# Optimization experiments

Measured on AMD Instinct MI355X. Metric: run time of the kernel, lower is better.

## Reference

```python
import jax, jax.numpy as jnp
import numpy as np

B, T, F = 256, 512, 64
H1, H2, OUT = 100, 128, 19


def setup_inputs() -> dict:
    key = jax.random.key(0)
    ks = jax.random.split(key, 6)
    s = 0.05  # small init so relu cell activation stays stable over 512 steps
    return {
        "x":  jax.random.normal(ks[0], (B, T, F), jnp.float32),
        "W1": jax.random.normal(ks[1], (F, 4 * H1), jnp.float32) * s,
        "U1": jax.random.normal(ks[2], (H1, 4 * H1), jnp.float32) * s,
        "b1": jnp.zeros((4 * H1,), jnp.float32),
        "W2": jax.random.normal(ks[3], (H1, 4 * H2), jnp.float32) * s,
        "U2": jax.random.normal(ks[4], (H2, 4 * H2), jnp.float32) * s,
        "b2": jnp.zeros((4 * H2,), jnp.float32),
        "Wd": jax.random.normal(ks[5], (H2, OUT), jnp.float32) * s,
        "bd": jnp.zeros((OUT,), jnp.float32),
    }


def _lstm_relu(x, W, U, b):
    """Keras LSTM with activation=relu, recurrent_activation=sigmoid.
    x: [B,T,F]. Returns full hidden sequence [B,T,H]. Gate order i,f,g,o."""
    H = U.shape[0]
    xproj = jnp.einsum('btf,fj->btj', x, W) + b  # [B,T,4H], input gemm hoisted out of scan

    def step(carry, xt):
        h, c = carry
        z = xt + h @ U                            # [B,4H]
        i, f, g, o = jnp.split(z, 4, axis=-1)
        i = jax.nn.sigmoid(i)
        f = jax.nn.sigmoid(f)
        g = jax.nn.relu(g)
        o = jax.nn.sigmoid(o)
        c = f * c + i * g
        h = o * jax.nn.relu(c)
        return (h, c), h

    h0 = jnp.zeros((x.shape[0], H), x.dtype)
    c0 = jnp.zeros_like(h0)
    _, hs = jax.lax.scan(step, (h0, c0), jnp.swapaxes(xproj, 0, 1))  # [T,B,H]
    return jnp.swapaxes(hs, 0, 1)


def reference(x, W1, U1, b1, W2, U2, b2, Wd, bd):
    h1 = _lstm_relu(x, W1, U1, b1)    # [B,T,H1] (return_sequences=True, stacked intent)
    h2 = _lstm_relu(h1, W2, U2, b2)   # [B,T,H2]
    last = h2[:, -1]                   # [B,H2] last timestep
    return jax.nn.softmax(last @ Wd + bd, axis=-1)
```

## Files before the change

### kernel.cpp

```cpp
#include <hip/hip_runtime.h>
#include <math.h>

#define B_   256
#define T_   512
#define F_   64
#define H1_  100
#define H2_  128
#define OUT_ 19
#define TCH  64
#define NCH  (T_/TCH)
#define NPC  512
#define KP   128

typedef unsigned int uint;
typedef _Float16 h16;
typedef __attribute__((ext_vector_type(2))) _Float16 h16x2;
typedef __attribute__((ext_vector_type(8))) _Float16 f16x8;
typedef __attribute__((ext_vector_type(4))) float f32x4;

#define XPW_BYTES (16ull*TCH*NPC*16*2)
#define H1G_BYTES (16ull*TCH*KP*16*2)
#define CST_BYTES (16ull*KP*16*4)
#define HST_BYTES (16ull*KP*16*2)
#define UF_BYTES  (128ull*64*8*2)

#define A_XP1A  0ull
#define A_XP1B  (A_XP1A + XPW_BYTES)
#define A_XP2A  (A_XP1B + XPW_BYTES)
#define A_XP2B  (A_XP2A + XPW_BYTES)
#define A_H1GA  (A_XP2B + XPW_BYTES)
#define A_H1GB  (A_H1GA + H1G_BYTES)
#define A_C1    (A_H1GB + H1G_BYTES)
#define A_C2    (A_C1   + CST_BYTES)
#define A_H1S   (A_C2   + CST_BYTES)
#define A_H2S   (A_H1S  + HST_BYTES)
#define A_U1F   (A_H2S  + HST_BYTES)
#define A_U2F   (A_U1F  + UF_BYTES)
#define WS_A    (A_U2F  + UF_BYTES)

#define B_XP1A  0ull
#define B_XP1B  (B_XP1A + XPW_BYTES)
#define B_XP2   (B_XP1B + XPW_BYTES)
#define B_H1G   (B_XP2  + XPW_BYTES)
#define B_C1    (B_H1G  + H1G_BYTES)
#define B_C2    (B_C1   + CST_BYTES)
#define B_H1S   (B_C2   + CST_BYTES)
#define B_H2S   (B_H1S  + HST_BYTES)
#define B_U1F   (B_H2S  + HST_BYTES)
#define B_U2F   (B_U1F  + UF_BYTES)
#define WS_B    (B_U2F  + UF_BYTES)

__device__ __forceinline__ float sigm(float x) { return 1.0f / (1.0f + __expf(-x)); }

__device__ __forceinline__ uint pk2(float a, float b) {
    h16x2 h; h.x = (h16)a; h.y = (h16)b;
    return __builtin_bit_cast(uint, h);
}

__device__ __forceinline__ f32x4 mfma16(f16x8 a, f16x8 b, f32x4 c) {
    return __builtin_amdgcn_mfma_f32_16x16x32_f16(a, b, c, 0, 0, 0);
}

__device__ __forceinline__ f32x4 up4(uint2 v) {
    h16x2 a = __builtin_bit_cast(h16x2, v.x);
    h16x2 b = __builtin_bit_cast(h16x2, v.y);
    f32x4 r; r[0] = (float)a.x; r[1] = (float)a.y; r[2] = (float)b.x; r[3] = (float)b.y;
    return r;
}

__device__ __forceinline__ void bar_lgkm() {
    asm volatile("s_waitcnt lgkmcnt(0)" ::: "memory");
    __builtin_amdgcn_sched_barrier(0);
    __builtin_amdgcn_s_barrier();
    __builtin_amdgcn_sched_barrier(0);
}

__device__ __forceinline__ f16x8 load_bfrag(const float* __restrict__ P, int H, int OG,
                                            int Kreal, int ubase, int g, int q, int lane) {
    const int u  = ubase + (lane & 15);
    const int k0 = q * 32 + (lane >> 4) * 8;
    const int col = g * H + u;
    float f[8];
    #pragma unroll
    for (int e = 0; e < 8; ++e) {
        const int k = k0 + e;
        f[e] = (u < H && k < Kreal) ? P[(size_t)k * OG + col] : 0.0f;
    }
    uint4 r;
    r.x = pk2(f[0], f[1]); r.y = pk2(f[2], f[3]);
    r.z = pk2(f[4], f[5]); r.w = pk2(f[6], f[7]);
    return __builtin_bit_cast(f16x8, r);
}

__global__ __launch_bounds__(512) void k_prepack(
    const float* __restrict__ U1, const float* __restrict__ U2,
    h16* __restrict__ U1f, h16* __restrict__ U2f)
{
    const int w = blockIdx.x & 7;
    const int layer = blockIdx.x >> 3;
    const float* U = layer ? U2 : U1;
    const int H = layer ? H2_ : H1_;
    h16* Uf = layer ? U2f : U1f;
    const int lane = threadIdx.x & 63;
    #pragma unroll
    for (int it = 0; it < 2; ++it) {
        const int combo = it * 8 + (threadIdx.x >> 6);
        const int g = combo >> 2, q = combo & 3;
        f16x8 fr = load_bfrag(U, H, 4 * H, H, w * 16, g, q, lane);
        *(f16x8*)(Uf + (size_t)(((w * 4 + g) * 4 + q) * 64 + lane) * 8) = fr;
    }
}

template<int MODE, int NIT>
__device__ __forceinline__ void dense_body(
    const float* __restrict__ Af, const h16* __restrict__ Ah,
    const float* __restrict__ W, const float* __restrict__ bias,
    const int H, const int ch, h16* __restrict__ xp,
    const int bid, const int j)
{
    const int lane = j & 63, w = j >> 6;
    const int KF = MODE ? 4 : 2;
    const int KREAL = MODE ? 100 : 64;
    const int OG = 4 * H;

    f16x8 bf[4][4];
    #pragma unroll
    for (int g = 0; g < 4; ++g)
        #pragma unroll
        for (int q = 0; q < 4; ++q)
            if (q < KF) bf[g][q] = load_bfrag(W, H, OG, KREAL, w * 16, g, q, lane);

    float bv[4];
    #pragma unroll
    for (int g = 0; g < 4; ++g) {
        const int u = w * 16 + (lane & 15);
        bv[g] = (u < H) ? bias[g * H + u] : 0.0f;
    }

    const int ci = lane & 15, hi = lane >> 4;
    #pragma unroll
    for (int it = 0; it < NIT; ++it) {
        const int m = bid * NIT + it;
        const int bt = m / TCH, tc = m % TCH;

        f16x8 af[4];
        if (MODE == 0) {
            const int b = bt * 16 + ci;
            const int t = ch * TCH + tc;
            #pragma unroll
            for (int q = 0; q < 2; ++q) {
                const int k0 = q * 32 + hi * 8;
                const float* p = Af + ((size_t)b * T_ + t) * F_ + k0;
                float4 x0 = *(const float4*)p;
                float4 x1 = *(const float4*)(p + 4);
                uint4 r;
                r.x = pk2(x0.x, x0.y); r.y = pk2(x0.z, x0.w);
                r.z = pk2(x1.x, x1.y); r.w = pk2(x1.z, x1.w);
                af[q] = __builtin_bit_cast(f16x8, r);
            }
        } else {
            #pragma unroll
            for (int q = 0; q < 4; ++q) {
                const int k0 = q * 32 + hi * 8;
                const size_t base = ((size_t)(bt * TCH + tc) * KP + k0) * 16 + ci;
                f16x8 a;
                #pragma unroll
                for (int e = 0; e < 8; ++e) a[e] = Ah[base + (size_t)e * 16];
                af[q] = a;
            }
        }

        f32x4 acc[4];
        #pragma unroll
        for (int g = 0; g < 4; ++g) { acc[g][0]=bv[g]; acc[g][1]=bv[g]; acc[g][2]=bv[g]; acc[g][3]=bv[g]; }
        #pragma unroll
        for (int g = 0; g < 4; ++g)
            #pragma unroll
            for (int q = 0; q < 4; ++q)
                if (q < KF) acc[g] = mfma16(af[q], bf[g][q], acc[g]);

        #pragma unroll
        for (int g = 0; g < 4; ++g) {
            const int c = (w * 4 + g) * 16 + ci;
            const size_t o = ((size_t)(bt * TCH + tc) * NPC + c) * 16 + hi * 4;
            uint2 s;
            s.x = pk2(acc[g][0], acc[g][1]);
            s.y = pk2(acc[g][2], acc[g][3]);
            *(uint2*)(xp + o) = s;
        }
    }
}

template<int MODE, int NIT>
__global__ __launch_bounds__(512) void k_dense(
    const float* __restrict__ Af, const h16* __restrict__ Ah,
    const float* __restrict__ W, const float* __restrict__ bias,
    const int H, const int ch, h16* __restrict__ xp)
{
    dense_body<MODE, NIT>(Af, Ah, W, bias, H, ch, xp, blockIdx.x, threadIdx.x);
}

#define LF(G,Q) f16x8 wf##G##Q = *(const f16x8*)(Uf + (size_t)(((w*4+G)*4+Q)*64 + lane)*8);

#define RSTEP(Pn, tcur)                                                          \
    {                                                                            \
        const int t_ = (tcur);                                                   \
        const h16* hb = &hbuf[t_ & 1][0][0];                                     \
        f16x8 a0 = *(const f16x8*)(hb + ci * 136 + 0  + hi * 8);                 \
        f16x8 a1 = *(const f16x8*)(hb + ci * 136 + 32 + hi * 8);                 \
        f16x8 a2 = *(const f16x8*)(hb + ci * 136 + 64 + hi * 8);                 \
        f16x8 a3 = *(const f16x8*)(hb + ci * 136 + 96 + hi * 8);                 \
        f32x4 z0 = up4(Pn##0), z1 = up4(Pn##1), z2 = up4(Pn##2), z3 = up4(Pn##3);\
        const uint to_ = (uint)((t_ + 2 < TCH) ? t_ + 2 : t_) * xstep;           \
        Pn##0 = *(const uint2*)(xp + xb0 + to_);                                 \
        Pn##1 = *(const uint2*)(xp + xb1 + to_);                                 \
        Pn##2 = *(const uint2*)(xp + xb2 + to_);                                 \
        Pn##3 = *(const uint2*)(xp + xb3 + to_);                                 \
        z0 = mfma16(a0, wf00, z0); z0 = mfma16(a1, wf01, z0);                    \
        z0 = mfma16(a2, wf02, z0); z0 = mfma16(a3, wf03, z0);                    \
        z1 = mfma16(a0, wf10, z1); z1 = mfma16(a1, wf11, z1);                    \
        z1 = mfma16(a2, wf12, z1); z1 = mfma16(a3, wf13, z1);                    \
        z2 = mfma16(a0, wf20, z2); z2 = mfma16(a1, wf21, z2);                    \
        z2 = mfma16(a2, wf22, z2); z2 = mfma16(a3, wf23, z2);                    \
        z3 = mfma16(a0, wf30, z3); z3 = mfma16(a1, wf31, z3);                    \
        z3 = mfma16(a2, wf32, z3); z3 = mfma16(a3, wf33, z3);                    \
        f32x4 hv;                                                                \
        _Pragma("unroll")                                                        \
        for (int i = 0; i < 4; ++i) {                                            \
            float ig = sigm(z0[i]);                                              \
            float fg = sigm(z1[i]);                                              \
            float gg = fmaxf(z2[i], 0.0f);                                       \
            float og = sigm(z3[i]);                                              \
            c[i] = fg * c[i] + ig * gg;                                          \
            hv[i] = og * fmaxf(c[i], 0.0f);                                      \
        }                                                                        \
        h16 h0 = (h16)hv[0], h1 = (h16)hv[1], h2 = (h16)hv[2], h3 = (h16)hv[3]; \
        const int nb_ = (t_ & 1) ^ 1;                                            \
        hbuf[nb_][r0 + 0][myu] = h0;                                             \
        hbuf[nb_][r0 + 1][myu] = h1;                                             \
        hbuf[nb_][r0 + 2][myu] = h2;                                             \
        hbuf[nb_][r0 + 3][myu] = h3;                                             \
        h16x2 p01_; p01_.x = h0; p01_.y = h1;                                    \
        h16x2 p23_; p23_.x = h2; p23_.y = h3;                                    \
        hp.x = __builtin_bit_cast(uint, p01_);                                   \
        hp.y = __builtin_bit_cast(uint, p23_);                                   \
        if (do_hout) *(uint2*)(hout + hob + (uint)t_ * hstep) = hp;              \
        bar_lgkm();                                                              \
    }

__device__ __forceinline__ void rec_body(
    const h16* __restrict__ Uf,
    const h16* __restrict__ xp, h16* __restrict__ hout, const int do_hout,
    float* __restrict__ cstate, h16* __restrict__ hstate, const int ch,
    const int bt, const int j)
{
    __shared__ h16 hbuf[2][16][136];
    const int lane = j & 63, w = j >> 6;
    const int ci = lane & 15, hi = lane >> 4;
    const int myu = w * 16 + ci;
    const int r0 = hi * 4;

    LF(0,0) LF(0,1) LF(0,2) LF(0,3)
    LF(1,0) LF(1,1) LF(1,2) LF(1,3)
    LF(2,0) LF(2,1) LF(2,2) LF(2,3)
    LF(3,0) LF(3,1) LF(3,2) LF(3,3)

    {
        const int u = j & 127, rr = (j >> 7) * 4;
        #pragma unroll
        for (int i = 0; i < 4; ++i) {
            h16 v = (h16)0.0f;
            if (ch != 0) v = hstate[((size_t)bt * KP + u) * 16 + rr + i];
            hbuf[0][rr + i][u] = v;
        }
    }
    f32x4 c;
    const size_t coff = ((size_t)bt * KP + myu) * 16 + r0;
    if (ch == 0) { c[0]=0.f; c[1]=0.f; c[2]=0.f; c[3]=0.f; }
    else         { c = *(const f32x4*)(cstate + coff); }
    __syncthreads();

    const uint xstep = NPC * 16;
    const uint xb0 = (uint)(((size_t)bt * TCH) * NPC + (w * 64 + ci)) * 16 + r0;
    const uint xb1 = xb0 + 16 * 16, xb2 = xb0 + 32 * 16, xb3 = xb0 + 48 * 16;

    uint2 pA0 = *(const uint2*)(xp + xb0);
    uint2 pA1 = *(const uint2*)(xp + xb1);
    uint2 pA2 = *(const uint2*)(xp + xb2);
    uint2 pA3 = *(const uint2*)(xp + xb3);
    uint2 pB0 = *(const uint2*)(xp + xb0 + xstep);
    uint2 pB1 = *(const uint2*)(xp + xb1 + xstep);
    uint2 pB2 = *(const uint2*)(xp + xb2 + xstep);
    uint2 pB3 = *(const uint2*)(xp + xb3 + xstep);

    const uint hstep = KP * 16;
    const uint hob = (uint)(((size_t)bt * TCH) * KP + myu) * 16 + r0;

    uint2 hp; hp.x = 0u; hp.y = 0u;

    for (int tt = 0; tt < TCH; tt += 2) {
        RSTEP(pA, tt)
        RSTEP(pB, tt + 1)
    }

    *(f32x4*)(cstate + coff) = c;
    *(uint2*)(hstate + ((size_t)bt * KP + myu) * 16 + r0) = hp;
}

__global__ __launch_bounds__(512) void k_mega(
    const int rec2_on, const h16* __restrict__ Uf2, const h16* __restrict__ xp2r,
    float* __restrict__ c2, h16* __restrict__ hs2, const int ch2,
    const int rec1_on, const h16* __restrict__ Uf1, const h16* __restrict__ xp1r,
    h16* __restrict__ h1gw, float* __restrict__ c1, h16* __restrict__ hs1, const int ch1,
    const int d2_on, const h16* __restrict__ h1gr, const float* __restrict__ W2,
    const float* __restrict__ b2, h16* __restrict__ xp2w,
    const int d1_on, const float* __restrict__ x, const float* __restrict__ W1,
    const float* __restrict__ b1, const int chd1, h16* __restrict__ xp1w)
{
    const int bid = blockIdx.x, j = threadIdx.x;
    if (bid < 16) {
        if (rec2_on) rec_body(Uf2, xp2r, (h16*)nullptr, 0, c2, hs2, ch2, bid, j);
    } else if (bid < 32) {
        if (rec1_on) rec_body(Uf1, xp1r, h1gw, 1, c1, hs1, ch1, bid - 16, j);
    } else if (bid < 288) {
        if (d2_on) dense_body<1, 4>((const float*)nullptr, h1gr, W2, b2, H2_, 0, xp2w, bid - 32, j);
    } else {
        if (d1_on) dense_body<0, 4>(x, (const h16*)nullptr, W1, b1, H1_, chd1, xp1w, bid - 288, j);
    }
}

__global__ void k_head(const h16* __restrict__ h2s, const float* __restrict__ Wd,
                       const float* __restrict__ bd, float* __restrict__ out)
{
    __shared__ float lg[OUT_];
    const int b = blockIdx.x, j = threadIdx.x;
    const int bt = b >> 4, r = b & 15;
    if (j < OUT_) {
        float acc = bd[j];
        for (int u = 0; u < H2_; ++u)
            acc += (float)h2s[((size_t)bt * KP + u) * 16 + r] * Wd[u * OUT_ + j];
        lg[j] = acc;
    }
    __syncthreads();
    if (j < OUT_) {
        float m = -1e30f;
        for (int k = 0; k < OUT_; ++k) m = fmaxf(m, lg[k]);
        float s = 0.0f;
        for (int k = 0; k < OUT_; ++k) s += expf(lg[k] - m);
        out[b * OUT_ + j] = expf(lg[j] - m) / s;
    }
}

#define G1_  400
#define G2_  512
#define FBTC 32
#define FB_XP1  0
#define FB_XP2  0
#define FB_WQ   51200
#define FB_XS   134400
#define FB_W2Q  32768
#define FB_H1C  139264
#define FB_U2Q  32768
#define FB_ZBUF 160000
#define FB_H1PK 162048
#define FB_H2PK 162256
#define FB_H2F  162512
#define FB_LDS  163328

__device__ __forceinline__ float fd2(uint wv, uint hv, float cc) {
#if __has_builtin(__builtin_amdgcn_fdot2)
    return __builtin_amdgcn_fdot2(__builtin_bit_cast(h16x2, wv),
                                  __builtin_bit_cast(h16x2, hv), cc, false);
#else
    h16x2 a = __builtin_bit_cast(h16x2, wv), b = __builtin_bit_cast(h16x2, hv);
    return cc + (float)a.x * (float)b.x + (float)a.y * (float)b.y;
#endif
}

__device__ __forceinline__ void stage_quads(const float* __restrict__ P, const int G,
                                            const int NQ, const int KREAL,
                                            char* dst, const int j)
{
    if (j < G) {
        for (int q = 0; q < NQ; ++q) {
            float f[8];
            #pragma unroll
            for (int r = 0; r < 8; ++r) {
                const int k = 8 * q + r;
                f[r] = (k < KREAL) ? P[(size_t)k * G + j] : 0.0f;
            }
            uint4 u;
            u.x = pk2(f[0], f[1]); u.y = pk2(f[2], f[3]);
            u.z = pk2(f[4], f[5]); u.w = pk2(f[6], f[7]);
            *(uint4*)(dst + (size_t)(q * G + j) * 16) = u;
        }
    }
}

__global__ __launch_bounds__(512) void lstm_fallback(
    const float* __restrict__ x,
    const float* __restrict__ W1, const float* __restrict__ U1, const float* __restrict__ b1,
    const float* __restrict__ W2, const float* __restrict__ U2, const float* __restrict__ b2,
    const float* __restrict__ Wd, const float* __restrict__ bd,
    float* __restrict__ out)
{
    __shared__ uint4 smem4[FB_LDS / 16];
    char* sm = (char*)smem4;
    const int b = blockIdx.x;
    const int j = threadIdx.x;
    float c1 = 0.0f, c2 = 0.0f;

    const uint u2r0 = pk2(U2[120 * G2_ + j], U2[121 * G2_ + j]);
    const uint u2r1 = pk2(U2[122 * G2_ + j], U2[123 * G2_ + j]);
    const uint u2r2 = pk2(U2[124 * G2_ + j], U2[125 * G2_ + j]);
    const uint u2r3 = pk2(U2[126 * G2_ + j], U2[127 * G2_ + j]);

    if (j < 52) *(uint*)(sm + FB_H1PK + 4 * j) = 0u;
    if (j < 64) *(uint*)(sm + FB_H2PK + 4 * j) = 0u;
    __syncthreads();

    const float* xrow = x + (size_t)b * T_ * F_;
    for (int ch = 0; ch < T_ / FBTC; ++ch) {
        stage_quads(W1, G1_, 8, 64, sm + FB_WQ, j);
        #pragma unroll
        for (int r = 0; r < 2; ++r) {
            int v = r * 512 + j;
            float2 xv = *(const float2*)(xrow + ch * (FBTC * F_) + 2 * v);
            *(uint*)(sm + FB_XS + 4 * v) = pk2(xv.x, xv.y);
        }
        __syncthreads();
        if (j < G1_) {
            const float bj = b1[j];
            const uint4* WQ = (const uint4*)(sm + FB_WQ);
            for (int t = 0; t < FBTC; ++t) {
                const uint4* XQ = (const uint4*)(sm + FB_XS + t * 128);
                float a0 = bj, a1 = 0.f, a2 = 0.f, a3 = 0.f;
                #pragma unroll
                for (int q = 0; q < 8; ++q) {
                    uint4 wq = WQ[q * G1_ + j]; uint4 hq = XQ[q];
                    a0 = fd2(wq.x, hq.x, a0); a1 = fd2(wq.y, hq.y, a1);
                    a2 = fd2(wq.z, hq.z, a2); a3 = fd2(wq.w, hq.w, a3);
                }
                *(float*)(sm + FB_XP1 + 4 * (t * G1_ + j)) = (a0 + a1) + (a2 + a3);
            }
        }
        __syncthreads();
        stage_quads(U1, G1_, 13, H1_, sm + FB_WQ, j);
        __syncthreads();
        for (int t = 0; t < FBTC; ++t) {
            if (j < G1_) {
                const uint4* WQ = (const uint4*)(sm + FB_WQ);
                const uint4* HP = (const uint4*)(sm + FB_H1PK);
                float a0 = *(const float*)(sm + FB_XP1 + 4 * (t * G1_ + j));
                float a1 = 0.f, a2 = 0.f, a3 = 0.f;
                #pragma unroll
                for (int q = 0; q < 13; ++q) {
                    uint4 wq = WQ[q * G1_ + j]; uint4 hq = HP[q];
                    a0 = fd2(wq.x, hq.x, a0); a1 = fd2(wq.y, hq.y, a1);
                    a2 = fd2(wq.z, hq.z, a2); a3 = fd2(wq.w, hq.w, a3);
                }
                *(float*)(sm + FB_ZBUF + 4 * j) = (a0 + a1) + (a2 + a3);
            }
            __syncthreads();
            if (j < H1_) {
                const float* zb = (const float*)(sm + FB_ZBUF);
                float ig = sigm(zb[j]);
                float fg = sigm(zb[H1_ + j]);
                float gg = fmaxf(zb[2 * H1_ + j], 0.0f);
                float og = sigm(zb[3 * H1_ + j]);
                c1 = fg * c1 + ig * gg;
                float h = og * fmaxf(c1, 0.0f);
                h16 hh = (h16)h;
                *(h16*)(sm + FB_H1PK + 2 * j) = hh;
                *(h16*)(sm + FB_H1C + t * 208 + 2 * j) = hh;
            }
            __syncthreads();
        }
        stage_quads(W2, G2_, 13, H1_, sm + FB_W2Q, j);
        __syncthreads();
        {
            const float bj = b2[j];
            const uint4* WQ = (const uint4*)(sm + FB_W2Q);
            for (int t = 0; t < FBTC; ++t) {
                const uint4* HC = (const uint4*)(sm + FB_H1C + t * 208);
                float a0 = bj, a1 = 0.f, a2 = 0.f, a3 = 0.f;
                #pragma unroll
                for (int q = 0; q < 13; ++q) {
                    uint4 wq = WQ[q * G2_ + j]; uint4 hq = HC[q];
                    a0 = fd2(wq.x, hq.x, a0); a1 = fd2(wq.y, hq.y, a1);
                    a2 = fd2(wq.z, hq.z, a2); a3 = fd2(wq.w, hq.w, a3);
                }
                *(h16*)(sm + FB_XP2 + 2 * (t * G2_ + j)) = (h16)((a0 + a1) + (a2 + a3));
            }
        }
        __syncthreads();
        stage_quads(U2, G2_, 15, 120, sm + FB_U2Q, j);
        __syncthreads();
        for (int t = 0; t < FBTC; ++t) {
            {
                const uint4* WQ = (const uint4*)(sm + FB_U2Q);
                const uint4* HP = (const uint4*)(sm + FB_H2PK);
                float a0 = (float)*(const h16*)(sm + FB_XP2 + 2 * (t * G2_ + j));
                float a1 = 0.f, a2 = 0.f, a3 = 0.f;
                #pragma unroll
                for (int q = 0; q < 15; ++q) {
                    uint4 wq = WQ[q * G2_ + j]; uint4 hq = HP[q];
                    a0 = fd2(wq.x, hq.x, a0); a1 = fd2(wq.y, hq.y, a1);
                    a2 = fd2(wq.z, hq.z, a2); a3 = fd2(wq.w, hq.w, a3);
                }
                uint4 hp15 = ((const uint4*)(sm + FB_H2PK))[15];
                a0 = fd2(u2r0, hp15.x, a0); a1 = fd2(u2r1, hp15.y, a1);
                a2 = fd2(u2r2, hp15.z, a2); a3 = fd2(u2r3, hp15.w, a3);
                *(float*)(sm + FB_ZBUF + 4 * j) = (a0 + a1) + (a2 + a3);
            }
            __syncthreads();
            if (j < H2_) {
                const float* zb = (const float*)(sm + FB_ZBUF);
                float ig = sigm(zb[j]);
                float fg = sigm(zb[H2_ + j]);
                float gg = fmaxf(zb[2 * H2_ + j], 0.0f);
                float og = sigm(zb[3 * H2_ + j]);
                c2 = fg * c2 + ig * gg;
                float h = og * fmaxf(c2, 0.0f);
                *(h16*)(sm + FB_H2PK + 2 * j) = (h16)h;
                *(float*)(sm + FB_H2F + 4 * j) = h;
            }
            __syncthreads();
        }
    }
    if (j < OUT_) {
        const float* h2 = (const float*)(sm + FB_H2F);
        float acc = bd[j];
        #pragma unroll
        for (int k = 0; k < H2_; ++k) acc += h2[k] * Wd[k * OUT_ + j];
        *(float*)(sm + FB_ZBUF + 4 * j) = acc;
    }
    __syncthreads();
    if (j < OUT_) {
        const float* zb = (const float*)(sm + FB_ZBUF);
        float m = -1e30f;
        for (int k = 0; k < OUT_; ++k) m = fmaxf(m, zb[k]);
        float s = 0.0f;
        for (int k = 0; k < OUT_; ++k) s += expf(zb[k] - m);
        out[b * OUT_ + j] = expf(zb[j] - m) / s;
    }
}

extern "C" void kernel_launch(void* const* d_in, const int* in_sizes, int n_in,
                              void* d_out, int out_size, void* d_ws, size_t ws_size,
                              hipStream_t stream) {
    const float* x  = (const float*)d_in[0];
    const float* W1 = (const float*)d_in[1];
    const float* U1 = (const float*)d_in[2];
    const float* b1 = (const float*)d_in[3];
    const float* W2 = (const float*)d_in[4];
    const float* U2 = (const float*)d_in[5];
    const float* b2 = (const float*)d_in[6];
    const float* Wd = (const float*)d_in[7];
    const float* bd = (const float*)d_in[8];
    float* out = (float*)d_out;

    if (ws_size >= WS_A) {
        char* ws = (char*)d_ws;
        h16* xp1[2] = { (h16*)(ws + A_XP1A), (h16*)(ws + A_XP1B) };
        h16* xp2[2] = { (h16*)(ws + A_XP2A), (h16*)(ws + A_XP2B) };
        h16* h1g[2] = { (h16*)(ws + A_H1GA), (h16*)(ws + A_H1GB) };
        float* c1  = (float*)(ws + A_C1);
        float* c2  = (float*)(ws + A_C2);
        h16*   hs1 = (h16*)(ws + A_H1S);
        h16*   hs2 = (h16*)(ws + A_H2S);
        h16*   u1f = (h16*)(ws + A_U1F);
        h16*   u2f = (h16*)(ws + A_U2F);

        k_prepack<<<16, 512, 0, stream>>>(U1, U2, u1f, u2f);
        k_dense<0, 4><<<256, 512, 0, stream>>>(x, (const h16*)nullptr, W1, b1, H1_, 0, xp1[0]);
        k_mega<<<544, 512, 0, stream>>>(
            0, u2f, (const h16*)nullptr, c2, hs2, 0,
            1, u1f, xp1[0], h1g[0], c1, hs1, 0,
            0, (const h16*)nullptr, W2, b2, (h16*)nullptr,
            1, x, W1, b1, 1, xp1[1]);
        k_mega<<<544, 512, 0, stream>>>(
            0, u2f, (const h16*)nullptr, c2, hs2, 0,
            1, u1f, xp1[1], h1g[1], c1, hs1, 1,
            1, h1g[0], W2, b2, xp2[0],
            1, x, W1, b1, 2, xp1[0]);
        for (int ch = 0; ch < NCH; ++ch) {
            const int r1on = (ch + 2 < NCH);
            const int d2on = (ch + 1 < NCH);
            const int d1on = (ch + 3 < NCH);
            k_mega<<<544, 512, 0, stream>>>(
                1, u2f, xp2[ch & 1], c2, hs2, ch,
                r1on, u1f, xp1[(ch + 2) & 1], h1g[(ch + 2) & 1], c1, hs1, ch + 2,
                d2on, h1g[(ch + 1) & 1], W2, b2, xp2[(ch + 1) & 1],
                d1on, x, W1, b1, ch + 3, xp1[(ch + 3) & 1]);
        }
        k_head<<<256, 64, 0, stream>>>(hs2, Wd, bd, out);
    } else if (ws_size >= WS_B) {
        char* ws = (char*)d_ws;
        h16* xp1[2] = { (h16*)(ws + B_XP1A), (h16*)(ws + B_XP1B) };
        h16*   xp2 = (h16*)(ws + B_XP2);
        h16*   h1g = (h16*)(ws + B_H1G);
        float* c1  = (float*)(ws + B_C1);
        float* c2  = (float*)(ws + B_C2);
        h16*   hs1 = (h16*)(ws + B_H1S);
        h16*   hs2 = (h16*)(ws + B_H2S);
        h16*   u1f = (h16*)(ws + B_U1F);
        h16*   u2f = (h16*)(ws + B_U2F);

        k_prepack<<<16, 512, 0, stream>>>(U1, U2, u1f, u2f);
        k_dense<0, 4><<<256, 512, 0, stream>>>(x, (const h16*)nullptr, W1, b1, H1_, 0, xp1[0]);
        k_mega<<<544, 512, 0, stream>>>(
            0, u2f, (const h16*)nullptr, c2, hs2, 0,
            1, u1f, xp1[0], h1g, c1, hs1, 0,
            0, (const h16*)nullptr, W2, b2, (h16*)nullptr,
            1, x, W1, b1, 1, xp1[1]);
        for (int ch = 0; ch < NCH; ++ch) {
            k_mega<<<288, 512, 0, stream>>>(
                0, u2f, (const h16*)nullptr, c2, hs2, 0,
                0, u1f, (const h16*)nullptr, (h16*)nullptr, c1, hs1, 0,
                1, h1g, W2, b2, xp2,
                0, x, W1, b1, 0, (h16*)nullptr);
            if (ch + 1 < NCH) {
                const int d1on = (ch + 2 < NCH);
                k_mega<<<544, 512, 0, stream>>>(
                    1, u2f, xp2, c2, hs2, ch,
                    1, u1f, xp1[(ch + 1) & 1], h1g, c1, hs1, ch + 1,
                    0, (const h16*)nullptr, W2, b2, (h16*)nullptr,
                    d1on, x, W1, b1, ch + 2, xp1[ch & 1]);
            } else {
                k_mega<<<16, 512, 0, stream>>>(
                    1, u2f, xp2, c2, hs2, ch,
                    0, u1f, (const h16*)nullptr, (h16*)nullptr, c1, hs1, 0,
                    0, (const h16*)nullptr, W2, b2, (h16*)nullptr,
                    0, x, W1, b1, 0, (h16*)nullptr);
            }
        }
        k_head<<<256, 64, 0, stream>>>(hs2, Wd, bd, out);
    } else {
        lstm_fallback<<<B_, 512, 0, stream>>>(x, W1, U1, b1, W2, U2, b2, Wd, bd, out);
    }
}
```

Baseline: 795.1 us.

## Fuse layer-2 input projection into layer-1 recurrence blocks and prepack W fragments

```diff
diff --git a/kernel.cpp b/kernel.cpp
--- a/kernel.cpp
+++ b/kernel.cpp
@@ -28,27 +28,16 @@
 #define A_XP1B  (A_XP1A + XPW_BYTES)
 #define A_XP2A  (A_XP1B + XPW_BYTES)
 #define A_XP2B  (A_XP2A + XPW_BYTES)
-#define A_H1GA  (A_XP2B + XPW_BYTES)
-#define A_H1GB  (A_H1GA + H1G_BYTES)
-#define A_C1    (A_H1GB + H1G_BYTES)
+#define A_H1G   (A_XP2B + XPW_BYTES)
+#define A_C1    (A_H1G  + H1G_BYTES)
 #define A_C2    (A_C1   + CST_BYTES)
 #define A_H1S   (A_C2   + CST_BYTES)
 #define A_H2S   (A_H1S  + HST_BYTES)
 #define A_U1F   (A_H2S  + HST_BYTES)
 #define A_U2F   (A_U1F  + UF_BYTES)
-#define WS_A    (A_U2F  + UF_BYTES)
-
-#define B_XP1A  0ull
-#define B_XP1B  (B_XP1A + XPW_BYTES)
-#define B_XP2   (B_XP1B + XPW_BYTES)
-#define B_H1G   (B_XP2  + XPW_BYTES)
-#define B_C1    (B_H1G  + H1G_BYTES)
-#define B_C2    (B_C1   + CST_BYTES)
-#define B_H1S   (B_C2   + CST_BYTES)
-#define B_H2S   (B_H1S  + HST_BYTES)
-#define B_U1F   (B_H2S  + HST_BYTES)
-#define B_U2F   (B_U1F  + UF_BYTES)
-#define WS_B    (B_U2F  + UF_BYTES)
+#define A_W1F   (A_U2F  + UF_BYTES)
+#define A_W2F   (A_W1F  + UF_BYTES)
+#define WS_A    (A_W2F  + UF_BYTES)
 
 __device__ __forceinline__ float sigm(float x) { return 1.0f / (1.0f + __expf(-x)); }
 
@@ -92,43 +81,48 @@
     return __builtin_bit_cast(f16x8, r);
 }
 
-__global__ __launch_bounds__(512) void k_prepack(
+__global__ __launch_bounds__(512) void k_prepack4(
     const float* __restrict__ U1, const float* __restrict__ U2,
-    h16* __restrict__ U1f, h16* __restrict__ U2f)
+    const float* __restrict__ W1, const float* __restrict__ W2,
+    h16* __restrict__ u1f, h16* __restrict__ u2f,
+    h16* __restrict__ w1f, h16* __restrict__ w2f)
 {
     const int w = blockIdx.x & 7;
-    const int layer = blockIdx.x >> 3;
-    const float* U = layer ? U2 : U1;
-    const int H = layer ? H2_ : H1_;
-    h16* Uf = layer ? U2f : U1f;
+    const int which = blockIdx.x >> 3;
+    const float* P; int H, K, KF; h16* D;
+    if (which == 0)      { P = U1; H = H1_; K = H1_; KF = 4; D = u1f; }
+    else if (which == 1) { P = U2; H = H2_; K = H2_; KF = 4; D = u2f; }
+    else if (which == 2) { P = W1; H = H1_; K = 64;  KF = 2; D = w1f; }
+    else                 { P = W2; H = H2_; K = H1_; KF = 4; D = w2f; }
     const int lane = threadIdx.x & 63;
     #pragma unroll
     for (int it = 0; it < 2; ++it) {
         const int combo = it * 8 + (threadIdx.x >> 6);
         const int g = combo >> 2, q = combo & 3;
-        f16x8 fr = load_bfrag(U, H, 4 * H, H, w * 16, g, q, lane);
-        *(f16x8*)(Uf + (size_t)(((w * 4 + g) * 4 + q) * 64 + lane) * 8) = fr;
-    }
-}
-
-template<int MODE, int NIT>
+        if (q < KF) {
+            f16x8 fr = load_bfrag(P, H, 4 * H, K, w * 16, g, q, lane);
+            *(f16x8*)(D + (size_t)(((w * 4 + g) * 4 + q) * 64 + lane) * 8) = fr;
+        }
+    }
+}
+
+template<int MODE>
 __device__ __forceinline__ void dense_body(
     const float* __restrict__ Af, const h16* __restrict__ Ah,
-    const float* __restrict__ W, const float* __restrict__ bias,
+    const h16* __restrict__ Wf, const float* __restrict__ bias,
     const int H, const int ch, h16* __restrict__ xp,
-    const int bid, const int j)
+    const int bid, const int j, const int nit)
 {
     const int lane = j & 63, w = j >> 6;
     const int KF = MODE ? 4 : 2;
-    const int KREAL = MODE ? 100 : 64;
-    const int OG = 4 * H;
 
     f16x8 bf[4][4];
     #pragma unroll
     for (int g = 0; g < 4; ++g)
         #pragma unroll
         for (int q = 0; q < 4; ++q)
-            if (q < KF) bf[g][q] = load_bfrag(W, H, OG, KREAL, w * 16, g, q, lane);
+            if (q < KF)
+                bf[g][q] = *(const f16x8*)(Wf + (size_t)(((w * 4 + g) * 4 + q) * 64 + lane) * 8);
 
     float bv[4];
     #pragma unroll
@@ -138,9 +132,9 @@
     }
 
     const int ci = lane & 15, hi = lane >> 4;
-    #pragma unroll
-    for (int it = 0; it < NIT; ++it) {
-        const int m = bid * NIT + it;
+    #pragma unroll 2
+    for (int it = 0; it < nit; ++it) {
+        const int m = bid * nit + it;
         const int bt = m / TCH, tc = m % TCH;
 
         f16x8 af[4];
@@ -191,13 +185,13 @@
     }
 }
 
-template<int MODE, int NIT>
+template<int MODE>
 __global__ __launch_bounds__(512) void k_dense(
     const float* __restrict__ Af, const h16* __restrict__ Ah,
-    const float* __restrict__ W, const float* __restrict__ bias,
+    const h16* __restrict__ Wf, const float* __restrict__ bias,
     const int H, const int ch, h16* __restrict__ xp)
 {
-    dense_body<MODE, NIT>(Af, Ah, W, bias, H, ch, xp, blockIdx.x, threadIdx.x);
+    dense_body<MODE>(Af, Ah, Wf, bias, H, ch, xp, blockIdx.x, threadIdx.x, 4);
 }
 
 #define LF(G,Q) f16x8 wf##G##Q = *(const f16x8*)(Uf + (size_t)(((w*4+G)*4+Q)*64 + lane)*8);
@@ -307,25 +301,27 @@
     *(uint2*)(hstate + ((size_t)bt * KP + myu) * 16 + r0) = hp;
 }
 
-__global__ __launch_bounds__(512) void k_mega(
+__global__ __launch_bounds__(512) void k_mega_f(
     const int rec2_on, const h16* __restrict__ Uf2, const h16* __restrict__ xp2r,
     float* __restrict__ c2, h16* __restrict__ hs2, const int ch2,
     const int rec1_on, const h16* __restrict__ Uf1, const h16* __restrict__ xp1r,
-    h16* __restrict__ h1gw, float* __restrict__ c1, h16* __restrict__ hs1, const int ch1,
-    const int d2_on, const h16* __restrict__ h1gr, const float* __restrict__ W2,
-    const float* __restrict__ b2, h16* __restrict__ xp2w,
-    const int d1_on, const float* __restrict__ x, const float* __restrict__ W1,
+    h16* __restrict__ h1g, float* __restrict__ c1, h16* __restrict__ hs1, const int ch1,
+    const h16* __restrict__ w2f, const float* __restrict__ b2, h16* __restrict__ xp2w,
+    const int d1_on, const float* __restrict__ x, const h16* __restrict__ w1f,
     const float* __restrict__ b1, const int chd1, h16* __restrict__ xp1w)
 {
     const int bid = blockIdx.x, j = threadIdx.x;
     if (bid < 16) {
         if (rec2_on) rec_body(Uf2, xp2r, (h16*)nullptr, 0, c2, hs2, ch2, bid, j);
     } else if (bid < 32) {
-        if (rec1_on) rec_body(Uf1, xp1r, h1gw, 1, c1, hs1, ch1, bid - 16, j);
-    } else if (bid < 288) {
-        if (d2_on) dense_body<1, 4>((const float*)nullptr, h1gr, W2, b2, H2_, 0, xp2w, bid - 32, j);
+        if (rec1_on) {
+            const int bt = bid - 16;
+            rec_body(Uf1, xp1r, h1g, 1, c1, hs1, ch1, bt, j);
+            __syncthreads();
+            dense_body<1>((const float*)nullptr, h1g, w2f, b2, H2_, 0, xp2w, bt, j, TCH);
+        }
     } else {
-        if (d1_on) dense_body<0, 4>(x, (const h16*)nullptr, W1, b1, H1_, chd1, xp1w, bid - 288, j);
+        if (d1_on) dense_body<0>(x, (const h16*)nullptr, w1f, b1, H1_, chd1, xp1w, bid - 32, j, 4);
     }
 }
 
@@ -564,76 +560,31 @@
         char* ws = (char*)d_ws;
         h16* xp1[2] = { (h16*)(ws + A_XP1A), (h16*)(ws + A_XP1B) };
         h16* xp2[2] = { (h16*)(ws + A_XP2A), (h16*)(ws + A_XP2B) };
-        h16* h1g[2] = { (h16*)(ws + A_H1GA), (h16*)(ws + A_H1GB) };
+        h16*   h1g = (h16*)(ws + A_H1G);
         float* c1  = (float*)(ws + A_C1);
         float* c2  = (float*)(ws + A_C2);
         h16*   hs1 = (h16*)(ws + A_H1S);
         h16*   hs2 = (h16*)(ws + A_H2S);
         h16*   u1f = (h16*)(ws + A_U1F);
         h16*   u2f = (h16*)(ws + A_U2F);
-
-        k_prepack<<<16, 512, 0, stream>>>(U1, U2, u1f, u2f);
-        k_dense<0, 4><<<256, 512, 0, stream>>>(x, (const h16*)nullptr, W1, b1, H1_, 0, xp1[0]);
-        k_mega<<<544, 512, 0, stream>>>(
-            0, u2f, (const h16*)nullptr, c2, hs2, 0,
-            1, u1f, xp1[0], h1g[0], c1, hs1, 0,
-            0, (const h16*)nullptr, W2, b2, (h16*)nullptr,
-            1, x, W1, b1, 1, xp1[1]);
-        k_mega<<<544, 512, 0, stream>>>(
-            0, u2f, (const h16*)nullptr, c2, hs2, 0,
-            1, u1f, xp1[1], h1g[1], c1, hs1, 1,
-            1, h1g[0], W2, b2, xp2[0],
-            1, x, W1, b1, 2, xp1[0]);
-        for (int ch = 0; ch < NCH; ++ch) {
-            const int r1on = (ch + 2 < NCH);
-            const int d2on = (ch + 1 < NCH);
-            const int d1on = (ch + 3 < NCH);
-            k_mega<<<544, 512, 0, stream>>>(
-                1, u2f, xp2[ch & 1], c2, hs2, ch,
-                r1on, u1f, xp1[(ch + 2) & 1], h1g[(ch + 2) & 1], c1, hs1, ch + 2,
-                d2on, h1g[(ch + 1) & 1], W2, b2, xp2[(ch + 1) & 1],
-                d1on, x, W1, b1, ch + 3, xp1[(ch + 3) & 1]);
-        }
-        k_head<<<256, 64, 0, stream>>>(hs2, Wd, bd, out);
-    } else if (ws_size >= WS_B) {
-        char* ws = (char*)d_ws;
-        h16* xp1[2] = { (h16*)(ws + B_XP1A), (h16*)(ws + B_XP1B) };
-        h16*   xp2 = (h16*)(ws + B_XP2);
-        h16*   h1g = (h16*)(ws + B_H1G);
-        float* c1  = (float*)(ws + B_C1);
-        float* c2  = (float*)(ws + B_C2);
-        h16*   hs1 = (h16*)(ws + B_H1S);
-        h16*   hs2 = (h16*)(ws + B_H2S);
-        h16*   u1f = (h16*)(ws + B_U1F);
-        h16*   u2f = (h16*)(ws + B_U2F);
-
-        k_prepack<<<16, 512, 0, stream>>>(U1, U2, u1f, u2f);
-        k_dense<0, 4><<<256, 512, 0, stream>>>(x, (const h16*)nullptr, W1, b1, H1_, 0, xp1[0]);
-        k_mega<<<544, 512, 0, stream>>>(
+        h16*   w1f = (h16*)(ws + A_W1F);
+        h16*   w2f = (h16*)(ws + A_W2F);
+
+        k_prepack4<<<32, 512, 0, stream>>>(U1, U2, W1, W2, u1f, u2f, w1f, w2f);
+        k_dense<0><<<256, 512, 0, stream>>>(x, (const h16*)nullptr, w1f, b1, H1_, 0, xp1[0]);
+        k_mega_f<<<288, 512, 0, stream>>>(
             0, u2f, (const h16*)nullptr, c2, hs2, 0,
             1, u1f, xp1[0], h1g, c1, hs1, 0,
-            0, (const h16*)nullptr, W2, b2, (h16*)nullptr,
-            1, x, W1, b1, 1, xp1[1]);
+            w2f, b2, xp2[0],
+            1, x, w1f, b1, 1, xp1[1]);
         for (int ch = 0; ch < NCH; ++ch) {
-            k_mega<<<288, 512, 0, stream>>>(
-                0, u2f, (const h16*)nullptr, c2, hs2, 0,
-                0, u1f, (const h16*)nullptr, (h16*)nullptr, c1, hs1, 0,
-                1, h1g, W2, b2, xp2,
-                0, x, W1, b1, 0, (h16*)nullptr);
-            if (ch + 1 < NCH) {
-                const int d1on = (ch + 2 < NCH);
-                k_mega<<<544, 512, 0, stream>>>(
-                    1, u2f, xp2, c2, hs2, ch,
-                    1, u1f, xp1[(ch + 1) & 1], h1g, c1, hs1, ch + 1,
-                    0, (const h16*)nullptr, W2, b2, (h16*)nullptr,
-                    d1on, x, W1, b1, ch + 2, xp1[ch & 1]);
-            } else {
-                k_mega<<<16, 512, 0, stream>>>(
-                    1, u2f, xp2, c2, hs2, ch,
-                    0, u1f, (const h16*)nullptr, (h16*)nullptr, c1, hs1, 0,
-                    0, (const h16*)nullptr, W2, b2, (h16*)nullptr,
-                    0, x, W1, b1, 0, (h16*)nullptr);
-            }
+            const int r1on = (ch + 1 < NCH);
+            const int d1on = (ch + 2 < NCH);
+            k_mega_f<<<288, 512, 0, stream>>>(
+                1, u2f, xp2[ch & 1], c2, hs2, ch,
+                r1on, u1f, xp1[(ch + 1) & 1], h1g, c1, hs1, ch + 1,
+                w2f, b2, xp2[(ch + 1) & 1],
+                d1on, x, w1f, b1, ch + 2, xp1[ch & 1]);
         }
         k_head<<<256, 64, 0, stream>>>(hs2, Wd, bd, out);
     } else {
```

Result: slower. 1.166 ms (+46.7%).
